# Kernel tuning notes

Hardware: AMD Instinct MI355X
Metric: run time of the kernel (lower is better)

Reference implementation:

```python
import jax, jax.numpy as jnp
import numpy as np
import math

B, S, D, H = 2, 2048, 1024, 16
DK = D // H


def setup_inputs() -> dict:
    key = jax.random.key(0)
    ks = jax.random.split(key, 14)
    inp = {
        "query": jax.random.normal(ks[0], (B, S, D), dtype=jnp.float32),
        "key": jax.random.normal(ks[1], (B, S, D), dtype=jnp.float32),
        "value": jax.random.normal(ks[2], (B, S, D), dtype=jnp.float32),
        "group_prob": jax.random.uniform(ks[3], (B, S, S), dtype=jnp.float32),
        "mask": jax.random.randint(ks[4], (B, S), 0, 2, dtype=jnp.int32),
    }
    scale = 0.02
    inp["Wq"] = jax.random.normal(ks[5], (D, D), dtype=jnp.float32) * scale
    inp["bq"] = jnp.zeros((D,), dtype=jnp.float32)
    inp["Wk"] = jax.random.normal(ks[6], (D, D), dtype=jnp.float32) * scale
    inp["bk"] = jnp.zeros((D,), dtype=jnp.float32)
    inp["Wv"] = jax.random.normal(ks[7], (D, D), dtype=jnp.float32) * scale
    inp["bv"] = jnp.zeros((D,), dtype=jnp.float32)
    inp["Wo"] = jax.random.normal(ks[8], (D, D), dtype=jnp.float32) * scale
    inp["bo"] = jnp.zeros((D,), dtype=jnp.float32)
    return inp


def reference(query, key, value, group_prob, mask, Wq, bq, Wk, bk, Wv, bv, Wo, bo):
    b, s, d = query.shape
    # project and split heads: [B,S,D] -> [B,H,S,DK]
    def proj(x, W, bias):
        return (x @ W.T + bias).reshape(b, s, H, DK).transpose(0, 2, 1, 3)

    q = proj(query, Wq, bq)
    k = proj(key, Wk, bk)
    v = proj(value, Wv, bv)

    scores = jnp.einsum("bhqd,bhkd->bhqk", q, k) / math.sqrt(DK)  # [B,H,S,S]

    # combined mask: padding-row mask OR diagonal (always attend to self)
    eye = jnp.eye(s, dtype=jnp.int32)
    combined = mask[:, None, None, :] | eye[None, None, :, :]  # [B,1,S,S]
    scores = jnp.where(combined == 0, jnp.float32(-1e9), scores)

    p_attn = jax.nn.softmax(scores, axis=-1)
    p_attn = p_attn * group_prob[:, None, :, :]  # post-softmax group scaling

    x = jnp.einsum("bhqk,bhkd->bhqd", p_attn, v)  # [B,H,S,DK]
    x = x.transpose(0, 2, 1, 3).reshape(b, s, d)
    return x @ Wo.T + bo
```

## Files before the change

### kernel.cpp

```cpp
#include <hip/hip_runtime.h>
#include <hip/hip_bf16.h>
#include <stdint.h>

typedef __bf16 bf16x8 __attribute__((ext_vector_type(8)));
typedef float f32x4 __attribute__((ext_vector_type(4)));

#define QSCALE 0.1803368801111244f

__device__ __forceinline__ void gld16(const void* g, void* l) {
  __builtin_amdgcn_global_load_lds(
      (__attribute__((address_space(1))) void*)(uintptr_t)(g),
      (__attribute__((address_space(3))) void*)(l), 16, 0, 0);
}

struct CastArgs {
  const float* src[7];
  __bf16* dst[7];
  int n[7];
};

__global__ __launch_bounds__(256) void cast_bf16_kernel(CastArgs a) {
  const int t = blockIdx.y;
  const int i = (blockIdx.x * 256 + threadIdx.x) * 8;
  if (i >= a.n[t]) return;
  const float4* s = (const float4*)(a.src[t] + i);
  float4 v0 = s[0], v1 = s[1];
  bf16x8 o;
  o[0] = (__bf16)v0.x; o[1] = (__bf16)v0.y; o[2] = (__bf16)v0.z; o[3] = (__bf16)v0.w;
  o[4] = (__bf16)v1.x; o[5] = (__bf16)v1.y; o[6] = (__bf16)v1.z; o[7] = (__bf16)v1.w;
  *(bf16x8*)(a.dst[t] + i) = o;
}

struct QkvArgs {
  const __bf16* A[3];
  const __bf16* B[3];
  const float* bias[3];
  __bf16* out[3];
};

__global__ __launch_bounds__(256) void qkv_gemm(QkvArgs args) {
  __shared__ __align__(16) __bf16 As[128 * 32];
  __shared__ __align__(16) __bf16 Bs[128 * 32];
  const int tid = threadIdx.x;
  const int z = blockIdx.y;
  const int bx = blockIdx.x;
  const int m0 = (z < 2 ? (bx >> 3) : (bx & 7)) * 128;
  const int n0 = (z < 2 ? (bx & 7) : (bx >> 3)) * 128;
  const __bf16* A = args.A[z];
  const __bf16* B = args.B[z];
  const float* bias = args.bias[z];
  __bf16* out = args.out[z];
  const float scale = (z == 0) ? QSCALE : 1.0f;

  const int lane = tid & 63, wid = tid >> 6;
  const int wm = (wid & 1) * 64, wn = (wid >> 1) * 64;
  const int l16 = lane & 15, quad = lane >> 4;

  const int sc = (tid & 3) ^ ((tid >> 2) & 3);
  const __bf16* ga = A + (size_t)(m0 + (tid >> 2)) * 1024 + sc * 8;
  const __bf16* gb = B + (size_t)(n0 + (tid >> 2)) * 1024 + sc * 8;
  char* lA = (char*)As + tid * 16;
  char* lB = (char*)Bs + tid * 16;
  const int a_off = (wm + l16) * 64 + ((quad ^ (l16 & 3)) * 16);
  const int b_off = (wn + l16) * 64 + ((quad ^ (l16 & 3)) * 16);

  f32x4 acc[4][4] = {};

  for (int k0 = 0; k0 < 1024; k0 += 32) {
    __syncthreads();
    gld16(ga + k0, lA);
    gld16(ga + k0 + 64 * 1024, lA + 4096);
    gld16(gb + k0, lB);
    gld16(gb + k0 + 64 * 1024, lB + 4096);
    __syncthreads();
    bf16x8 af[4], bfr[4];
#pragma unroll
    for (int mi = 0; mi < 4; ++mi)
      af[mi] = *(const bf16x8*)((const char*)As + a_off + mi * 1024);
#pragma unroll
    for (int ni = 0; ni < 4; ++ni)
      bfr[ni] = *(const bf16x8*)((const char*)Bs + b_off + ni * 1024);
#pragma unroll
    for (int mi = 0; mi < 4; ++mi)
#pragma unroll
      for (int ni = 0; ni < 4; ++ni)
        acc[mi][ni] = __builtin_amdgcn_mfma_f32_16x16x32_bf16(af[mi], bfr[ni],
                                                              acc[mi][ni], 0, 0, 0);
  }

  if (z < 2) {
#pragma unroll
    for (int ni = 0; ni < 4; ++ni) {
      const int col = n0 + wn + ni * 16 + l16;
      const int h = col >> 6, dk = col & 63;
      const float bb = bias[col];
#pragma unroll
      for (int mi = 0; mi < 4; ++mi)
#pragma unroll
        for (int r = 0; r < 4; ++r) {
          const int row = m0 + wm + mi * 16 + quad * 4 + r;
          const int b = row >> 11, s = row & 2047;
          out[((size_t)(b * 16 + h) * 2048 + s) * 64 + dk] =
              (__bf16)((acc[mi][ni][r] + bb) * scale);
        }
    }
  } else {
#pragma unroll
    for (int mi = 0; mi < 4; ++mi)
#pragma unroll
      for (int r = 0; r < 4; ++r) {
        const int rowm = m0 + wm + mi * 16 + quad * 4 + r;
        const int h = rowm >> 6, dk = rowm & 63;
        const float bb = bias[rowm];
#pragma unroll
        for (int ni = 0; ni < 4; ++ni) {
          const int coln = n0 + wn + ni * 16 + l16;
          const int b = coln >> 11, s = coln & 2047;
          out[((size_t)(b * 16 + h) * 64 + dk) * 2048 + s] =
              (__bf16)(acc[mi][ni][r] + bb);
        }
      }
  }
}

__global__ __launch_bounds__(256) void gemm_out(const __bf16* __restrict__ A,
                                                const __bf16* __restrict__ B,
                                                const float* __restrict__ bias,
                                                float* __restrict__ out) {
  __shared__ __align__(16) __bf16 As[128 * 32];
  __shared__ __align__(16) __bf16 Bs[128 * 32];
  const int tid = threadIdx.x;
  const int m0 = blockIdx.y * 128;
  const int n0 = blockIdx.x * 128;
  const int lane = tid & 63, wid = tid >> 6;
  const int wm = (wid & 1) * 64, wn = (wid >> 1) * 64;
  const int l16 = lane & 15, quad = lane >> 4;

  const int sc = (tid & 3) ^ ((tid >> 2) & 3);
  const __bf16* ga = A + (size_t)(m0 + (tid >> 2)) * 1024 + sc * 8;
  const __bf16* gb = B + (size_t)(n0 + (tid >> 2)) * 1024 + sc * 8;
  char* lA = (char*)As + tid * 16;
  char* lB = (char*)Bs + tid * 16;
  const int a_off = (wm + l16) * 64 + ((quad ^ (l16 & 3)) * 16);
  const int b_off = (wn + l16) * 64 + ((quad ^ (l16 & 3)) * 16);

  f32x4 acc[4][4] = {};

  for (int k0 = 0; k0 < 1024; k0 += 32) {
    __syncthreads();
    gld16(ga + k0, lA);
    gld16(ga + k0 + 64 * 1024, lA + 4096);
    gld16(gb + k0, lB);
    gld16(gb + k0 + 64 * 1024, lB + 4096);
    __syncthreads();
    bf16x8 af[4], bfr[4];
#pragma unroll
    for (int mi = 0; mi < 4; ++mi)
      af[mi] = *(const bf16x8*)((const char*)As + a_off + mi * 1024);
#pragma unroll
    for (int ni = 0; ni < 4; ++ni)
      bfr[ni] = *(const bf16x8*)((const char*)Bs + b_off + ni * 1024);
#pragma unroll
    for (int mi = 0; mi < 4; ++mi)
#pragma unroll
      for (int ni = 0; ni < 4; ++ni)
        acc[mi][ni] = __builtin_amdgcn_mfma_f32_16x16x32_bf16(af[mi], bfr[ni],
                                                              acc[mi][ni], 0, 0, 0);
  }

#pragma unroll
  for (int ni = 0; ni < 4; ++ni) {
    const int col = n0 + wn + ni * 16 + l16;
    const float bb = bias[col];
#pragma unroll
    for (int mi = 0; mi < 4; ++mi)
#pragma unroll
      for (int r = 0; r < 4; ++r) {
        const int row = m0 + wm + mi * 16 + quad * 4 + r;
        out[(size_t)row * 1024 + col] = acc[mi][ni][r] + bb;
      }
  }
}

__global__ __launch_bounds__(512, 4) void attn_kernel(
    const __bf16* __restrict__ Qh, const __bf16* __restrict__ Kh,
    const __bf16* __restrict__ Vt, const float* __restrict__ gprob,
    const int* __restrict__ maskp, __bf16* __restrict__ xb) {
  __shared__ __align__(16) __bf16 Ks[2][64 * 64];
  __shared__ __align__(16) __bf16 Vs[2][64 * 64];
  __shared__ __align__(16) __bf16 Ps[8][16 * 64];
  __shared__ unsigned long long mbits[32];

  const int tid = threadIdx.x;
  const int qt = blockIdx.x, bh = blockIdx.y;
  const int b = bh >> 4, h = bh & 15;
  const int q0 = qt * 128;
  const int lane = tid & 63, wid = tid >> 6, l16 = lane & 15, quad = lane >> 4;
  const size_t head_off = (size_t)bh * (2048 * 64);

  const int srow = tid >> 3;
  const int sc8 = (tid & 7) ^ (srow & 7);
  const int fxor = (l16 & 7);

  const __bf16* gk0 = Kh + head_off + (size_t)srow * 64 + sc8 * 8;
  const __bf16* gv0 = Vt + head_off + (size_t)srow * 2048 + sc8 * 8;

  gld16(gk0, (char*)Ks + tid * 16);
  gld16(gv0, (char*)Vs + tid * 16);

  bf16x8 aq[2];
  {
    const __bf16* gq = Qh + head_off + (size_t)(q0 + wid * 16 + l16) * 64 + quad * 8;
    aq[0] = *(const bf16x8*)(gq);
    aq[1] = *(const bf16x8*)(gq + 32);
  }

  int irow[4];
#pragma unroll
  for (int r = 0; r < 4; ++r) irow[r] = q0 + wid * 16 + quad * 4 + r;

  const float* gpl = gprob + (size_t)b * 2048 * 2048 +
                     (size_t)(q0 + wid * 16 + l16) * 2048 + quad * 8;
  float4 g0 = *(const float4*)(gpl);
  float4 g1 = *(const float4*)(gpl + 4);
  float4 g2 = *(const float4*)(gpl + 32);
  float4 g3 = *(const float4*)(gpl + 36);

  {
    const int* mr = maskp + b * 2048;
#pragma unroll
    for (int t = 0; t < 4; ++t) {
      const int kt2 = wid * 4 + t;
      const int mv = mr[kt2 * 64 + lane];
      const unsigned long long bal = __ballot(mv != 0);
      if (lane == 0) mbits[kt2] = bal;
    }
  }
  __syncthreads();

  f32x4 o[4] = {};
  float lp[4] = {0.f, 0.f, 0.f, 0.f};

  const int dkt = qt * 2 + (wid >> 2);

  for (int kt = 0; kt < 32; ++kt) {
    const int cur = kt & 1;
    float4 gn0, gn1, gn2, gn3;
    if (kt < 31) {
      const int nb = cur ^ 1;
      gld16(gk0 + (kt + 1) * 4096, (char*)Ks + nb * 8192 + tid * 16);
      gld16(gv0 + (kt + 1) * 64, (char*)Vs + nb * 8192 + tid * 16);
      const float* gn = gpl + (kt + 1) * 64;
      gn0 = *(const float4*)(gn);
      gn1 = *(const float4*)(gn + 4);
      gn2 = *(const float4*)(gn + 32);
      gn3 = *(const float4*)(gn + 36);
    }

    const unsigned long long sh = mbits[kt] >> l16;
    const uint32_t shlo = (uint32_t)sh, shhi = (uint32_t)(sh >> 32);
    const bool mk[4] = {(shlo & 1) != 0, (shlo & 0x10000u) != 0,
                        (shhi & 1) != 0, (shhi & 0x10000u) != 0};

    f32x4 sc[4] = {};
#pragma unroll
    for (int kh = 0; kh < 2; ++kh)
#pragma unroll
      for (int ni = 0; ni < 4; ++ni) {
        bf16x8 bk = *(const bf16x8*)((const char*)Ks + cur * 8192 +
                                     (ni * 16 + l16) * 128 +
                                     (((kh * 4 + quad) ^ fxor) * 16));
        sc[ni] = __builtin_amdgcn_mfma_f32_16x16x32_bf16(aq[kh], bk, sc[ni], 0, 0, 0);
      }

    float pw[4][4];
    if (kt != dkt) {
#pragma unroll
      for (int ni = 0; ni < 4; ++ni)
#pragma unroll
        for (int r = 0; r < 4; ++r) {
          const float e = __builtin_exp2f(sc[ni][r]);
          const float p = mk[ni] ? e : 0.f;
          lp[r] += p;
          pw[ni][r] = p;
        }
    } else {
#pragma unroll
      for (int ni = 0; ni < 4; ++ni)
#pragma unroll
        for (int r = 0; r < 4; ++r) {
          const float e = __builtin_exp2f(sc[ni][r]);
          const bool diag = (ni == (wid & 3)) && (l16 == quad * 4 + r);
          const float p = (mk[ni] || diag) ? e : 0.f;
          lp[r] += p;
          pw[ni][r] = p;
        }
    }

#pragma unroll
    for (int ni = 0; ni < 4; ++ni)
#pragma unroll
      for (int r = 0; r < 4; ++r) {
        const int prow = quad * 4 + r;
        const int pchunk = (ni * 2 + (l16 >> 3)) ^ (prow & 7);
        *(__bf16*)((char*)&Ps[wid][0] + prow * 128 + pchunk * 16 + (l16 & 7) * 2) =
            (__bf16)pw[ni][r];
      }
    asm volatile("s_waitcnt lgkmcnt(0)" ::: "memory");

    const float gfl[16] = {g0.x, g0.y, g0.z, g0.w, g1.x, g1.y, g1.z, g1.w,
                           g2.x, g2.y, g2.z, g2.w, g3.x, g3.y, g3.z, g3.w};
#pragma unroll
    for (int kh = 0; kh < 2; ++kh) {
      bf16x8 ap = *(const bf16x8*)((const char*)&Ps[wid][0] + l16 * 128 +
                                   (((kh * 4 + quad) ^ fxor) * 16));
      bf16x8 apg;
#pragma unroll
      for (int j = 0; j < 8; ++j)
        apg[j] = (__bf16)((float)ap[j] * gfl[kh * 8 + j]);
#pragma unroll
      for (int ni = 0; ni < 4; ++ni) {
        bf16x8 bv = *(const bf16x8*)((const char*)Vs + cur * 8192 +
                                     (ni * 16 + l16) * 128 +
                                     (((kh * 4 + quad) ^ fxor) * 16));
        o[ni] = __builtin_amdgcn_mfma_f32_16x16x32_bf16(apg, bv, o[ni], 0, 0, 0);
      }
    }

    if (kt < 31) { g0 = gn0; g1 = gn1; g2 = gn2; g3 = gn3; }
    __syncthreads();
  }

#pragma unroll
  for (int r = 0; r < 4; ++r) {
    lp[r] += __shfl_xor(lp[r], 1);
    lp[r] += __shfl_xor(lp[r], 2);
    lp[r] += __shfl_xor(lp[r], 4);
    lp[r] += __shfl_xor(lp[r], 8);
    lp[r] = 1.f / lp[r];
  }
#pragma unroll
  for (int ni = 0; ni < 4; ++ni) {
    const int dk = ni * 16 + l16;
#pragma unroll
    for (int r = 0; r < 4; ++r) {
      const float val = o[ni][r] * lp[r];
      xb[((size_t)(b * 2048 + irow[r])) * 1024 + h * 64 + dk] = (__bf16)val;
    }
  }
}

extern "C" void kernel_launch(void* const* d_in, const int* in_sizes, int n_in,
                              void* d_out, int out_size, void* d_ws, size_t ws_size,
                              hipStream_t stream) {
  const float* query = (const float*)d_in[0];
  const float* key_  = (const float*)d_in[1];
  const float* value = (const float*)d_in[2];
  const float* gprob = (const float*)d_in[3];
  const int*   maskp = (const int*)d_in[4];
  const float* Wq = (const float*)d_in[5];
  const float* bq = (const float*)d_in[6];
  const float* Wk = (const float*)d_in[7];
  const float* bk = (const float*)d_in[8];
  const float* Wv = (const float*)d_in[9];
  const float* bv = (const float*)d_in[10];
  const float* Wo = (const float*)d_in[11];
  const float* bo = (const float*)d_in[12];

  char* ws = (char*)d_ws;
  const size_t MB = 1 << 20;
  __bf16* qb  = (__bf16*)(ws + 0 * MB);
  __bf16* kb  = (__bf16*)(ws + 8 * MB);
  __bf16* vb  = (__bf16*)(ws + 16 * MB);
  __bf16* Wqb = (__bf16*)(ws + 24 * MB);
  __bf16* Wkb = (__bf16*)(ws + 26 * MB);
  __bf16* Wvb = (__bf16*)(ws + 28 * MB);
  __bf16* Wob = (__bf16*)(ws + 30 * MB);
  __bf16* Qh  = (__bf16*)(ws + 32 * MB);
  __bf16* Kh  = (__bf16*)(ws + 40 * MB);
  __bf16* Vt  = (__bf16*)(ws + 48 * MB);
  __bf16* xb  = (__bf16*)(ws + 56 * MB);

  CastArgs ca;
  ca.src[0] = query; ca.dst[0] = qb;  ca.n[0] = 4194304;
  ca.src[1] = key_;  ca.dst[1] = kb;  ca.n[1] = 4194304;
  ca.src[2] = value; ca.dst[2] = vb;  ca.n[2] = 4194304;
  ca.src[3] = Wq;    ca.dst[3] = Wqb; ca.n[3] = 1048576;
  ca.src[4] = Wk;    ca.dst[4] = Wkb; ca.n[4] = 1048576;
  ca.src[5] = Wv;    ca.dst[5] = Wvb; ca.n[5] = 1048576;
  ca.src[6] = Wo;    ca.dst[6] = Wob; ca.n[6] = 1048576;
  cast_bf16_kernel<<<dim3(2048, 7), 256, 0, stream>>>(ca);

  QkvArgs qa;
  qa.A[0] = qb;  qa.B[0] = Wqb; qa.bias[0] = bq; qa.out[0] = Qh;
  qa.A[1] = kb;  qa.B[1] = Wkb; qa.bias[1] = bk; qa.out[1] = Kh;
  qa.A[2] = Wvb; qa.B[2] = vb;  qa.bias[2] = bv; qa.out[2] = Vt;
  qkv_gemm<<<dim3(256, 3), 256, 0, stream>>>(qa);

  attn_kernel<<<dim3(16, 32), 512, 0, stream>>>(Qh, Kh, Vt, gprob, maskp, xb);
  gemm_out<<<dim3(8, 32), 256, 0, stream>>>(xb, Wob, bo, (float*)d_out);
}
```

Baseline: 317.3 us.

## Compute transposed scores so P feeds PV MFMA from registers, drop LDS staging

```diff
diff --git a/kernel.cpp b/kernel.cpp
--- a/kernel.cpp
+++ b/kernel.cpp
@@ -188,7 +188,6 @@
     const int* __restrict__ maskp, __bf16* __restrict__ xb) {
   __shared__ __align__(16) __bf16 Ks[2][64 * 64];
   __shared__ __align__(16) __bf16 Vs[2][64 * 64];
-  __shared__ __align__(16) __bf16 Ps[8][16 * 64];
   __shared__ unsigned long long mbits[32];
 
   const int tid = threadIdx.x;
@@ -202,7 +201,10 @@
   const int sc8 = (tid & 7) ^ (srow & 7);
   const int fxor = (l16 & 7);
 
-  const __bf16* gk0 = Kh + head_off + (size_t)srow * 64 + sc8 * 8;
+  const int sig = ((srow & 16) << 1) + ((srow & 12) << 1) + ((srow & 32) >> 3) +
+                  (srow & 3);
+
+  const __bf16* gk0 = Kh + head_off + (size_t)sig * 64 + sc8 * 8;
   const __bf16* gv0 = Vt + head_off + (size_t)srow * 2048 + sc8 * 8;
 
   gld16(gk0, (char*)Ks + tid * 16);
@@ -239,9 +241,10 @@
   __syncthreads();
 
   f32x4 o[4] = {};
-  float lp[4] = {0.f, 0.f, 0.f, 0.f};
+  float lp = 0.f;
 
   const int dkt = qt * 2 + (wid >> 2);
+  const int kqbase = (wid & 3) * 16 + l16 - quad * 8;
 
   for (int kt = 0; kt < 32; ++kt) {
     const int cur = kt & 1;
@@ -257,12 +260,10 @@
       gn3 = *(const float4*)(gn + 36);
     }
 
-    const unsigned long long sh = mbits[kt] >> l16;
+    const unsigned long long sh = mbits[kt] >> (quad * 8);
     const uint32_t shlo = (uint32_t)sh, shhi = (uint32_t)(sh >> 32);
-    const bool mk[4] = {(shlo & 1) != 0, (shlo & 0x10000u) != 0,
-                        (shhi & 1) != 0, (shhi & 0x10000u) != 0};
-
-    f32x4 sc[4] = {};
+
+    f32x4 p2[4] = {};
 #pragma unroll
     for (int kh = 0; kh < 2; ++kh)
 #pragma unroll
@@ -270,60 +271,50 @@
         bf16x8 bk = *(const bf16x8*)((const char*)Ks + cur * 8192 +
                                      (ni * 16 + l16) * 128 +
                                      (((kh * 4 + quad) ^ fxor) * 16));
-        sc[ni] = __builtin_amdgcn_mfma_f32_16x16x32_bf16(aq[kh], bk, sc[ni], 0, 0, 0);
+        p2[ni] = __builtin_amdgcn_mfma_f32_16x16x32_bf16(bk, aq[kh], p2[ni], 0, 0, 0);
       }
 
-    float pw[4][4];
+    const float gfl[16] = {g0.x, g0.y, g0.z, g0.w, g1.x, g1.y, g1.z, g1.w,
+                           g2.x, g2.y, g2.z, g2.w, g3.x, g3.y, g3.z, g3.w};
+    bf16x8 pa0, pa1;
     if (kt != dkt) {
 #pragma unroll
       for (int ni = 0; ni < 4; ++ni)
 #pragma unroll
         for (int r = 0; r < 4; ++r) {
-          const float e = __builtin_exp2f(sc[ni][r]);
-          const float p = mk[ni] ? e : 0.f;
-          lp[r] += p;
-          pw[ni][r] = p;
+          const int j = ((ni >> 1) << 2) + r;
+          const float e = __builtin_exp2f(p2[ni][r]);
+          const bool mk = (((ni & 1) ? shhi : shlo) >> j) & 1;
+          const float em = mk ? e : 0.f;
+          lp += em;
+          const float pg = em * gfl[(ni & 1) * 8 + j];
+          if (ni & 1) pa1[j] = (__bf16)pg; else pa0[j] = (__bf16)pg;
         }
     } else {
 #pragma unroll
       for (int ni = 0; ni < 4; ++ni)
 #pragma unroll
         for (int r = 0; r < 4; ++r) {
-          const float e = __builtin_exp2f(sc[ni][r]);
-          const bool diag = (ni == (wid & 3)) && (l16 == quad * 4 + r);
-          const float p = (mk[ni] || diag) ? e : 0.f;
-          lp[r] += p;
-          pw[ni][r] = p;
+          const int j = ((ni >> 1) << 2) + r;
+          const float e = __builtin_exp2f(p2[ni][r]);
+          const bool mk = (((ni & 1) ? shhi : shlo) >> j) & 1;
+          const bool diag = (kqbase == ((ni & 1) * 32 + j));
+          const float em = (mk || diag) ? e : 0.f;
+          lp += em;
+          const float pg = em * gfl[(ni & 1) * 8 + j];
+          if (ni & 1) pa1[j] = (__bf16)pg; else pa0[j] = (__bf16)pg;
         }
     }
 
 #pragma unroll
-    for (int ni = 0; ni < 4; ++ni)
-#pragma unroll
-      for (int r = 0; r < 4; ++r) {
-        const int prow = quad * 4 + r;
-        const int pchunk = (ni * 2 + (l16 >> 3)) ^ (prow & 7);
-        *(__bf16*)((char*)&Ps[wid][0] + prow * 128 + pchunk * 16 + (l16 & 7) * 2) =
-            (__bf16)pw[ni][r];
-      }
-    asm volatile("s_waitcnt lgkmcnt(0)" ::: "memory");
-
-    const float gfl[16] = {g0.x, g0.y, g0.z, g0.w, g1.x, g1.y, g1.z, g1.w,
-                           g2.x, g2.y, g2.z, g2.w, g3.x, g3.y, g3.z, g3.w};
-#pragma unroll
     for (int kh = 0; kh < 2; ++kh) {
-      bf16x8 ap = *(const bf16x8*)((const char*)&Ps[wid][0] + l16 * 128 +
-                                   (((kh * 4 + quad) ^ fxor) * 16));
-      bf16x8 apg;
-#pragma unroll
-      for (int j = 0; j < 8; ++j)
-        apg[j] = (__bf16)((float)ap[j] * gfl[kh * 8 + j]);
+      const bf16x8 pa = kh ? pa1 : pa0;
 #pragma unroll
       for (int ni = 0; ni < 4; ++ni) {
         bf16x8 bv = *(const bf16x8*)((const char*)Vs + cur * 8192 +
                                      (ni * 16 + l16) * 128 +
                                      (((kh * 4 + quad) ^ fxor) * 16));
-        o[ni] = __builtin_amdgcn_mfma_f32_16x16x32_bf16(apg, bv, o[ni], 0, 0, 0);
+        o[ni] = __builtin_amdgcn_mfma_f32_16x16x32_bf16(pa, bv, o[ni], 0, 0, 0);
       }
     }
 
@@ -331,20 +322,17 @@
     __syncthreads();
   }
 
-#pragma unroll
-  for (int r = 0; r < 4; ++r) {
-    lp[r] += __shfl_xor(lp[r], 1);
-    lp[r] += __shfl_xor(lp[r], 2);
-    lp[r] += __shfl_xor(lp[r], 4);
-    lp[r] += __shfl_xor(lp[r], 8);
-    lp[r] = 1.f / lp[r];
-  }
+  lp += __shfl_xor(lp, 16);
+  lp += __shfl_xor(lp, 32);
+  float rinv[4];
+#pragma unroll
+  for (int r = 0; r < 4; ++r) rinv[r] = 1.f / __shfl(lp, quad * 4 + r);
 #pragma unroll
   for (int ni = 0; ni < 4; ++ni) {
     const int dk = ni * 16 + l16;
 #pragma unroll
     for (int r = 0; r < 4; ++r) {
-      const float val = o[ni][r] * lp[r];
+      const float val = o[ni][r] * rinv[r];
       xb[((size_t)(b * 2048 + irow[r])) * 1024 + h * 64 + dk] = (__bf16)val;
     }
   }
```

After: 301.9 us. 1.05x faster.
